# Kernel optimization log

Measured on AMD Instinct MI355X. Metric: run time of the kernel, lower is better.

## Reference

```python
import jax, jax.numpy as jnp
import numpy as np

B, N, D, P, DS = 64, 16, 64, 5, 32
M = N * (N - 1)
TEMP = (DS * P * P) ** 0.5


def conv2d(x, w, b):
    # NCHW conv, stride 1, padding==SAME for k=3/p=1 and k=1/p=0
    y = jax.lax.conv_general_dilated(x, w, (1, 1), 'SAME',
                                     dimension_numbers=('NCHW', 'OIHW', 'NCHW'))
    return y + b[None, :, None, None]


def setup_inputs() -> dict:
    key = jax.random.key(0)
    ks = jax.random.split(key, 10)
    w = lambda k, shape: jax.random.normal(k, shape, jnp.float32) * 0.02
    x = jax.random.normal(ks[0], (B, N, D, P, P), jnp.float32)
    # g_idx: all ordered pairs (i, j) with j != i, plus valid flag 1
    pairs = np.array([(i, j) for i in range(N) for j in range(N) if j != i], dtype=np.int64)
    g = np.concatenate([pairs, np.ones((M, 1), np.int64)], axis=1)  # [M,3]
    g_idx = jnp.tile(jnp.asarray(g)[None], (B, 1, 1))  # [B,M,3]
    return dict(
        x=x, g_idx=g_idx,
        w_rel=w(ks[1], (D, 2 * D, 3, 3)), b_rel=jnp.zeros((D,), jnp.float32),
        w_self=w(ks[2], (D, D, 3, 3)), b_self=jnp.zeros((D,), jnp.float32),
        w_aff=w(ks[3], (D, D, 3, 3)), b_aff=jnp.zeros((D,), jnp.float32),
        w_agg=w(ks[4], (D, 2 * D, 3, 3)), b_agg=jnp.zeros((D,), jnp.float32),
        w_attn=w(ks[5], (DS, D, 1, 1)), b_attn=jnp.zeros((DS,), jnp.float32),
        w_q=w(ks[6], (DS, DS, 3, 3)), b_q=jnp.zeros((DS,), jnp.float32),
        w_k=w(ks[7], (DS, DS, 3, 3)), b_k=jnp.zeros((DS,), jnp.float32),
        gamma=jnp.ones((N, D, P, P), jnp.float32),
        beta=jnp.zeros((N, D, P, P), jnp.float32),
    )


def reference(x, g_idx, w_rel, b_rel, w_self, b_self, w_aff, b_aff,
              w_agg, b_agg, w_attn, b_attn, w_q, b_q, w_k, b_k, gamma, beta):
    s = x
    bsz, n, d, p, _ = x.shape
    # pairwise gather: x1[b, m] == x[b, m % n]
    x1 = jnp.tile(x, (1, n - 1, 1, 1, 1))  # [B, M, D, P, P]
    bidx = jnp.arange(bsz)[:, None]
    y1 = x1[bidx, g_idx[:, :, 0]]  # [B, M, D, P, P]
    y2 = x1[bidx, g_idx[:, :, 1]]
    r = jnp.concatenate([y1, y2], axis=2)  # [B, M, 2D, P, P]
    r = r * g_idx[:, :, 2][:, :, None, None, None].astype(x.dtype)
    r = jax.nn.relu(conv2d(r.reshape(-1, 2 * d, p, p), w_rel, b_rel))
    r = r.reshape(bsz, n, n - 1, d, p, p)
    # attention over objects
    s2d = conv2d(s.reshape(-1, d, p, p), w_attn, b_attn)  # [B*N, DS, P, P]
    q = jax.nn.relu(conv2d(s2d, w_q, b_q)).reshape(bsz, n, -1)
    k = jax.nn.relu(conv2d(s2d, w_k, b_k)).reshape(bsz, n, -1)
    attn = jnp.einsum('bif,bjf->bij', q / TEMP, k)
    sm = jax.nn.softmax(attn, axis=-1)
    self_wts = jnp.diagonal(sm, axis1=1, axis2=2)  # [B, N]
    # off-diagonal weights, per row in ascending column order (matches torch bool-mask view)
    off = jnp.asarray(np.array([[j for j in range(n) if j != i] for i in range(n)], dtype=np.int64))
    rel_wts = jnp.take_along_axis(sm, off[None], axis=2)  # [B, N, N-1]
    r = (rel_wts[:, :, :, None, None, None] * r).sum(axis=2)  # [B, N, D, P, P]
    xs = jax.nn.relu(conv2d(x.reshape(-1, d, p, p), w_self, b_self)).reshape(bsz, n, d, p, p)
    pred = self_wts[:, :, None, None, None] * xs + r
    a = jax.nn.relu(conv2d(pred.reshape(-1, d, p, p), w_aff, b_aff)).reshape(bsz, n, d, p, p)
    a = a + s
    # LayerNorm over [N, D, P, P] per batch element
    mu = a.mean(axis=(1, 2, 3, 4), keepdims=True)
    var = a.var(axis=(1, 2, 3, 4), keepdims=True)
    a = (a - mu) / jnp.sqrt(var + 1e-6) * gamma[None] + beta[None]
    a = jnp.concatenate([a, s], axis=2)  # [B, N, 2D, P, P]
    out = jax.nn.relu(conv2d(a.reshape(-1, 2 * d, p, p), w_agg, b_agg)).reshape(bsz, n, d, p, p)
    return out
```

## Files before the change

### kernel.cpp

```cpp
#include <hip/hip_runtime.h>
#include <hip/hip_bf16.h>

#define DEV static __device__ __forceinline__

typedef short s8v __attribute__((ext_vector_type(8)));
typedef float f16v __attribute__((ext_vector_type(16)));
typedef unsigned short u16;
typedef unsigned int u32;

constexpr int IMG = 1024;
constexpr int IE  = 1600;
constexpr float INV_TEMP = 0.035355339059327376f;

constexpr int WU = 0, WV = 36864, WSELF = 73728, WAFF = 110592,
              WAGA = 147456, WAGS = 184320;
constexpr int WQ = 221184, WK = 230400;
constexpr size_t OFF_Q    = 119808;
constexpr size_t OFF_K    = OFF_Q + 819200;
constexpr size_t OFF_U    = OFF_Q;
constexpr size_t OFF_V    = OFF_Q + 1638400;
constexpr size_t OFF_XS   = OFF_V + 1638400;
constexpr size_t OFF_A    = OFF_XS + 1638400;
constexpr size_t OFF_SM   = OFF_A + 1638400;
constexpr size_t OFF_SUMS = OFF_SM + 16384;
constexpr size_t OFF_WTS  = OFF_SUMS + 128;

DEV u16 f2bf(float f) {
  u32 u = __float_as_uint(f);
  return (u16)((u + 0x7FFF + ((u >> 16) & 1)) >> 16);
}
DEV int xrow(int p) { return (p / 5 + 1) * 8 + (p % 5 + 1); }
DEV int slotOf(int R) { return (3 * (R >> 3) + (R & 7)) & 7; }
DEV f16v zero16() {
  f16v z;
#pragma unroll
  for (int i = 0; i < 16; ++i) z[i] = 0.f;
  return z;
}
DEV void xt_write_pair(u16* xt, int p, int cp, float v0, float v1) {
  int R = xrow(p);
  int chunk = ((cp >> 2) ^ slotOf(R)) & 7;
  u32 u = (u32)f2bf(v0) | ((u32)f2bf(v1) << 16);
  *(u32*)((char*)xt + R * 128 + chunk * 16 + (cp & 3) * 4) = u;
}
DEV void mk_bases(int lane, int bases[9]) {
  int p = lane & 31; if (p > 24) p = 24;
  int hi = lane >> 5;
  int y = p / 5, x = p % 5;
#pragma unroll
  for (int t = 0; t < 9; ++t) {
    int R = (y + t / 3) * 8 + (x + t % 3);
    int sl = slotOf(R);
    bases[t] = R * 128 + (((sl ^ hi) & 7) << 4);
  }
}

__global__ __launch_bounds__(256) void k0_prep(
    const float* __restrict__ w_rel, const float* __restrict__ w_self,
    const float* __restrict__ w_aff, const float* __restrict__ w_agg,
    const float* __restrict__ w_q, const float* __restrict__ w_k,
    const float* __restrict__ w_attn, float* __restrict__ ws) {
  u16* wb = (u16*)ws;
  int idx = blockIdx.x * 256 + threadIdx.x;
  if (idx < 221184) {
    int reg = idx / 36864, w = idx % 36864;
    int o = w / 576, k = w % 576, t = k >> 6, c = k & 63;
    float v;
    switch (reg) {
      case 0:  v = w_rel[(o * 128 + c) * 9 + t]; break;
      case 1:  v = w_rel[(o * 128 + 64 + c) * 9 + t]; break;
      case 2:  v = w_self[(o * 64 + c) * 9 + t]; break;
      case 3:  v = w_aff[(o * 64 + c) * 9 + t]; break;
      case 4:  v = w_agg[(o * 128 + c) * 9 + t]; break;
      default: v = w_agg[(o * 128 + 64 + c) * 9 + t]; break;
    }
    wb[idx] = f2bf(v);
  } else if (idx < 239616) {
    int i2 = idx - 221184;
    int conv = i2 / 9216, r = i2 % 9216;
    int o = r / 288, k = r % 288, t = k >> 5, c = k & 31;
    const float* src = conv ? w_k : w_q;
    wb[idx] = f2bf(src[(o * 32 + c) * 9 + t]);
  } else if (idx < 239616 + 2048) {
    int i2 = idx - 239616;
    int c = i2 >> 5, ds = i2 & 31;
    ws[OFF_WTS + i2] = w_attn[ds * 64 + c];
  }
}

__global__ __launch_bounds__(256, 2) void k1_qk(
    const float* __restrict__ x, const float* __restrict__ b_attn,
    const float* __restrict__ b_q, const float* __restrict__ b_k,
    float* __restrict__ ws) {
  __shared__ float xlin[3200];
  __shared__ float wts[2048];
  __shared__ u16 xt32[2 * 3584];
  const u16* wb = (const u16*)ws;
  int tid = threadIdx.x, lane = tid & 63, wave = tid >> 6, hi = lane >> 5;
  int img0 = blockIdx.x * 2;
  int conv = wave & 1, wimg = wave >> 1;
  int oA = lane & 31;
  const u16* wsrc = wb + (conv ? WK : WQ) + oA * 288 + hi * 8;
  s8v A[18];
#pragma unroll
  for (int s = 0; s < 18; ++s) A[s] = *(const s8v*)(wsrc + s * 16);
  int bases[9]; mk_bases(lane, bases);
  for (int i = tid; i < 3200; i += 256) xlin[i] = x[(size_t)img0 * IE + i];
  for (int i = tid; i < 2048; i += 256) wts[i] = ws[OFF_WTS + i];
  for (int i = tid; i < 3584; i += 256) ((u32*)xt32)[i] = 0;
  __syncthreads();
  if (tid < 200) {
    int im = tid / 100, r = tid % 100, dsg = r / 25, p = r % 25;
    float acc[8];
#pragma unroll
    for (int d = 0; d < 8; ++d) acc[d] = b_attn[dsg * 8 + d];
    const float* xp = &xlin[im * IE + p];
#pragma unroll 4
    for (int c = 0; c < 64; ++c) {
      float xv = xp[c * 25];
      const float* wp = &wts[c * 32 + dsg * 8];
#pragma unroll
      for (int d = 0; d < 8; ++d) acc[d] = fmaf(wp[d], xv, acc[d]);
    }
    s8v pk;
#pragma unroll
    for (int d = 0; d < 8; ++d) pk[d] = (short)f2bf(acc[d]);
    int R = xrow(p);
    int chunk = (dsg ^ slotOf(R)) & 7;
    *(s8v*)((char*)xt32 + im * 7168 + R * 128 + chunk * 16) = pk;
  }
  __syncthreads();
  f16v acc = zero16();
  const char* xb = (const char*)xt32 + wimg * 7168;
#pragma unroll
  for (int s = 0; s < 18; ++s) {
    s8v bfr = *(const s8v*)(xb + (bases[s >> 1] ^ ((s & 1) << 5)));
    acc = __builtin_amdgcn_mfma_f32_32x32x16_bf16(A[s], bfr, acc, 0, 0, 0);
  }
  float* outp = ws + (conv ? OFF_K : OFF_Q) + (size_t)(img0 + wimg) * 800;
  const float* bq = conv ? b_k : b_q;
  int p = lane & 31;
  if (p < 25) {
#pragma unroll
    for (int r = 0; r < 16; ++r) {
      int ol = (r & 3) + 8 * (r >> 2) + 4 * hi;
      outp[ol * 25 + p] = fmaxf(acc[r] + bq[ol], 0.f);
    }
  }
}

__global__ __launch_bounds__(256) void k2_attn(float* __restrict__ ws) {
  __shared__ float kb[16][804];
  __shared__ float att[16][17];
  __shared__ float rowm[16], rowsum[16];
  int b = blockIdx.x, tid = threadIdx.x;
  const float* kg = ws + OFF_K + (size_t)b * 12800;
  for (int i = tid; i < 12800; i += 256) kb[i / 800][i % 800] = kg[i];
  if (tid < 2) ws[OFF_SUMS + b * 2 + tid] = 0.f;
  __syncthreads();
  int i = tid >> 4, j = tid & 15;
  const float* qr = ws + OFF_Q + (size_t)(b * 16 + i) * 800;
  float acc = 0.f;
  for (int f = 0; f < 800; f += 4) {
    float4 a = *(const float4*)(qr + f);
    float4 c = *(const float4*)&kb[j][f];
    acc += a.x * c.x + a.y * c.y + a.z * c.z + a.w * c.w;
  }
  att[i][j] = acc * INV_TEMP;
  __syncthreads();
  if (tid < 16) {
    float m = att[tid][0];
    for (int jj = 1; jj < 16; ++jj) m = fmaxf(m, att[tid][jj]);
    float s = 0.f;
    for (int jj = 0; jj < 16; ++jj) s += expf(att[tid][jj] - m);
    rowm[tid] = m; rowsum[tid] = 1.f / s;
  }
  __syncthreads();
  ws[OFF_SM + (size_t)b * 256 + tid] = expf(att[i][j] - rowm[i]) * rowsum[i];
}

__global__ __launch_bounds__(384, 2) void k3_uvxs(
    const float* __restrict__ x, const float* __restrict__ b_rel,
    const float* __restrict__ b_self, float* __restrict__ ws) {
  __shared__ float xlin[1600];
  __shared__ u16 xt[3584];
  const u16* wb = (const u16*)ws;
  int tid = threadIdx.x, lane = tid & 63, wave = tid >> 6, hi = lane >> 5;
  int conv = wave >> 1, ot = wave & 1;
  int oA = ot * 32 + (lane & 31);
  const u16* wsrc = wb + (conv == 0 ? WU : (conv == 1 ? WV : WSELF)) + oA * 576 + hi * 8;
  s8v A[36];
#pragma unroll
  for (int s = 0; s < 36; ++s) A[s] = *(const s8v*)(wsrc + s * 16);
  int bases[9]; mk_bases(lane, bases);
  for (int i = tid; i < 1792; i += 384) ((u32*)xt)[i] = 0;
  int img0 = blockIdx.x * 4;
  size_t obase = conv == 0 ? OFF_U : (conv == 1 ? OFF_V : OFF_XS);
  for (int im = 0; im < 4; ++im) {
    int img = img0 + im;
    __syncthreads();
    for (int i = tid; i < 1600; i += 384) xlin[i] = x[(size_t)img * IE + i];
    __syncthreads();
    for (int i = tid; i < 800; i += 384) {
      int p = i >> 5, cp = i & 31;
      xt_write_pair(xt, p, cp, xlin[cp * 50 + p], xlin[cp * 50 + 25 + p]);
    }
    __syncthreads();
    f16v acc = zero16();
#pragma unroll
    for (int s = 0; s < 36; ++s) {
      s8v bfr = *(const s8v*)((const char*)xt + (bases[s >> 2] ^ ((s & 3) << 5)));
      acc = __builtin_amdgcn_mfma_f32_32x32x16_bf16(A[s], bfr, acc, 0, 0, 0);
    }
    int p = lane & 31;
    if (p < 25) {
      float* outp = ws + obase + (size_t)img * IE;
#pragma unroll
      for (int r = 0; r < 16; ++r) {
        int ol = ot * 32 + (r & 3) + 8 * (r >> 2) + 4 * hi;
        float v = acc[r];
        if (conv == 1) v += b_rel[ol];
        if (conv == 2) v = fmaxf(v + b_self[ol], 0.f);
        outp[ol * 25 + p] = v;
      }
    }
  }
}

__global__ __launch_bounds__(256, 2) void k5_pred_aff(
    const float* __restrict__ x, const float* __restrict__ b_aff,
    float* __restrict__ ws) {
  __shared__ float predlin[2][1600];
  __shared__ u16 xt[2][3584];
  __shared__ float smr[2][16];
  __shared__ float selfw[2];
  const u16* wb = (const u16*)ws;
  int tid = threadIdx.x, lane = tid & 63, wave = tid >> 6, hi = lane >> 5;
  int img0 = blockIdx.x * 2, bat = img0 >> 4;
  int wimg = wave >> 1, ot = wave & 1;
  int oA = ot * 32 + (lane & 31);
  const u16* wsrc = wb + WAFF + oA * 576 + hi * 8;
  s8v A[36];
#pragma unroll
  for (int s = 0; s < 36; ++s) A[s] = *(const s8v*)(wsrc + s * 16);
  int bases[9]; mk_bases(lane, bases);
  for (int i = tid; i < 3584; i += 256) ((u32*)&xt[0][0])[i] = 0;
  if (tid < 32) { int k = tid >> 4, j = tid & 15; smr[k][j] = ws[OFF_SM + (size_t)(img0 + k) * 16 + j]; }
  if (tid < 2)  { int n = (img0 + tid) & 15; selfw[tid] = ws[OFF_SM + (size_t)(img0 + tid) * 16 + n]; }
  __syncthreads();
  const float* U = ws + OFF_U; const float* V = ws + OFF_V; const float* XS = ws + OFF_XS;
  for (int i4 = tid; i4 < 800; i4 += 256) {
    int im = i4 / 400, e = (i4 % 400) * 4;
    size_t gi = (size_t)(img0 + im) * IE + e;
    float4 uu = *(const float4*)(U + gi);
    float4 xx = *(const float4*)(XS + gi);
    float sw = selfw[im];
    int nk = (img0 + im) & 15;
    float ax = sw * xx.x, ay = sw * xx.y, az = sw * xx.z, aw = sw * xx.w;
#pragma unroll
    for (int j = 0; j < 16; ++j) {
      float wj = (j == nk) ? 0.f : smr[im][j];
      float4 vv = *(const float4*)(V + (size_t)(bat * 16 + j) * IE + e);
      ax = fmaf(wj, fmaxf(uu.x + vv.x, 0.f), ax);
      ay = fmaf(wj, fmaxf(uu.y + vv.y, 0.f), ay);
      az = fmaf(wj, fmaxf(uu.z + vv.z, 0.f), az);
      aw = fmaf(wj, fmaxf(uu.w + vv.w, 0.f), aw);
    }
    *(float4*)&predlin[im][e] = make_float4(ax, ay, az, aw);
  }
  __syncthreads();
  for (int i = tid; i < 1600; i += 256) {
    int im = i / 800, r = i % 800, p = r >> 5, cp = r & 31;
    xt_write_pair(&xt[im][0], p, cp, predlin[im][cp * 50 + p], predlin[im][cp * 50 + 25 + p]);
  }
  __syncthreads();
  f16v acc = zero16();
  const char* xb = (const char*)&xt[wimg][0];
#pragma unroll
  for (int s = 0; s < 36; ++s) {
    s8v bfr = *(const s8v*)(xb + (bases[s >> 2] ^ ((s & 3) << 5)));
    acc = __builtin_amdgcn_mfma_f32_32x32x16_bf16(A[s], bfr, acc, 0, 0, 0);
  }
  int p = lane & 31;
  float s1 = 0.f, s2 = 0.f;
  float* aout = ws + OFF_A + (size_t)(img0 + wimg) * IE;
  const float* xg = x + (size_t)(img0 + wimg) * IE;
  if (p < 25) {
#pragma unroll
    for (int r = 0; r < 16; ++r) {
      int ol = ot * 32 + (r & 3) + 8 * (r >> 2) + 4 * hi;
      float a = fmaxf(acc[r] + b_aff[ol], 0.f) + xg[ol * 25 + p];
      aout[ol * 25 + p] = a;
      s1 += a; s2 = fmaf(a, a, s2);
    }
  }
  for (int off = 32; off; off >>= 1) {
    s1 += __shfl_down(s1, off, 64);
    s2 += __shfl_down(s2, off, 64);
  }
  if (lane == 0) {
    atomicAdd(ws + OFF_SUMS + bat * 2, s1);
    atomicAdd(ws + OFF_SUMS + bat * 2 + 1, s2);
  }
}

__global__ __launch_bounds__(256, 2) void k6_agg(
    const float* __restrict__ x, const float* __restrict__ gamma,
    const float* __restrict__ beta, const float* __restrict__ b_agg,
    float* __restrict__ ws, float* __restrict__ out) {
  __shared__ float alin[2][1600];
  __shared__ float xlin[2][1600];
  __shared__ u16 xta[2][3584];
  __shared__ u16 xtx[2][3584];
  __shared__ float pbuf[4][1024];
  const u16* wb = (const u16*)ws;
  int tid = threadIdx.x, lane = tid & 63, wave = tid >> 6, hi = lane >> 5;
  int img0 = blockIdx.x * 2, bat = img0 >> 4;
  int ot = wave >> 1, h = wave & 1;
  int oA = ot * 32 + (lane & 31);
  const u16* wsrc = wb + (h ? WAGS : WAGA) + oA * 576 + hi * 8;
  s8v A[36];
#pragma unroll
  for (int s = 0; s < 36; ++s) A[s] = *(const s8v*)(wsrc + s * 16);
  int bases[9]; mk_bases(lane, bases);
  float ssum = ws[OFF_SUMS + bat * 2], ssq = ws[OFF_SUMS + bat * 2 + 1];
  float mu = ssum * (1.f / 25600.f);
  float var = ssq * (1.f / 25600.f) - mu * mu;
  float rstd = rsqrtf(var + 1e-6f);
  for (int i = tid; i < 3584; i += 256) { ((u32*)&xta[0][0])[i] = 0; ((u32*)&xtx[0][0])[i] = 0; }
  float* al = &alin[0][0]; float* xl = &xlin[0][0];
  const float* ag = ws + OFF_A + (size_t)img0 * IE;
  const float* xg = x + (size_t)img0 * IE;
  for (int i = tid; i < 3200; i += 256) { al[i] = ag[i]; xl[i] = xg[i]; }
  __syncthreads();
  for (int i = tid; i < 1600; i += 256) {
    int im = i / 800, r = i % 800, p = r >> 5, cp = r & 31;
    int n = (img0 + im) & 15;
    int e0 = cp * 50 + p, e1 = e0 + 25;
    float a0 = al[im * 1600 + e0], a1 = al[im * 1600 + e1];
    float an0 = (a0 - mu) * rstd * gamma[(size_t)n * IE + e0] + beta[(size_t)n * IE + e0];
    float an1 = (a1 - mu) * rstd * gamma[(size_t)n * IE + e1] + beta[(size_t)n * IE + e1];
    xt_write_pair(&xta[im][0], p, cp, an0, an1);
    xt_write_pair(&xtx[im][0], p, cp, xl[im * 1600 + e0], xl[im * 1600 + e1]);
  }
  __syncthreads();
  const char* bsrc = h ? (const char*)&xtx[0][0] : (const char*)&xta[0][0];
  f16v acc0 = zero16(), acc1 = zero16();
#pragma unroll
  for (int s = 0; s < 36; ++s) {
    s8v bfr = *(const s8v*)(bsrc + (bases[s >> 2] ^ ((s & 3) << 5)));
    acc0 = __builtin_amdgcn_mfma_f32_32x32x16_bf16(A[s], bfr, acc0, 0, 0, 0);
  }
#pragma unroll
  for (int s = 0; s < 36; ++s) {
    s8v bfr = *(const s8v*)(bsrc + 7168 + (bases[s >> 2] ^ ((s & 3) << 5)));
    acc1 = __builtin_amdgcn_mfma_f32_32x32x16_bf16(A[s], bfr, acc1, 0, 0, 0);
  }
  int p = lane & 31;
  if (h == 1) {
#pragma unroll
    for (int r = 0; r < 16; ++r) {
      int ol = (r & 3) + 8 * (r >> 2) + 4 * hi;
      pbuf[0 + ot][ol * 32 + p] = acc0[r];
      pbuf[2 + ot][ol * 32 + p] = acc1[r];
    }
  }
  __syncthreads();
  if (h == 0 && p < 25) {
#pragma unroll
    for (int r = 0; r < 16; ++r) {
      int ol = (r & 3) + 8 * (r >> 2) + 4 * hi;
      int o = ot * 32 + ol;
      float v0 = acc0[r] + pbuf[0 + ot][ol * 32 + p] + b_agg[o];
      float v1 = acc1[r] + pbuf[2 + ot][ol * 32 + p] + b_agg[o];
      out[(size_t)(img0 + 0) * IE + o * 25 + p] = fmaxf(v0, 0.f);
      out[(size_t)(img0 + 1) * IE + o * 25 + p] = fmaxf(v1, 0.f);
    }
  }
}

extern "C" void kernel_launch(void* const* d_in, const int* in_sizes, int n_in,
                              void* d_out, int out_size, void* d_ws,
                              size_t ws_size, hipStream_t stream) {
  const float* x      = (const float*)d_in[0];
  const float* w_rel  = (const float*)d_in[2];
  const float* b_rel  = (const float*)d_in[3];
  const float* w_self = (const float*)d_in[4];
  const float* b_self = (const float*)d_in[5];
  const float* w_aff  = (const float*)d_in[6];
  const float* b_aff  = (const float*)d_in[7];
  const float* w_agg  = (const float*)d_in[8];
  const float* b_agg  = (const float*)d_in[9];
  const float* w_attn = (const float*)d_in[10];
  const float* b_attn = (const float*)d_in[11];
  const float* w_q    = (const float*)d_in[12];
  const float* b_q    = (const float*)d_in[13];
  const float* w_k    = (const float*)d_in[14];
  const float* b_k    = (const float*)d_in[15];
  const float* gamma  = (const float*)d_in[16];
  const float* beta   = (const float*)d_in[17];
  float* ws  = (float*)d_ws;
  float* out = (float*)d_out;

  k0_prep<<<944, 256, 0, stream>>>(w_rel, w_self, w_aff, w_agg, w_q, w_k, w_attn, ws);
  k1_qk<<<IMG / 2, 256, 0, stream>>>(x, b_attn, b_q, b_k, ws);
  k2_attn<<<64, 256, 0, stream>>>(ws);
  k3_uvxs<<<IMG / 4, 384, 0, stream>>>(x, b_rel, b_self, ws);
  k5_pred_aff<<<IMG / 2, 256, 0, stream>>>(x, b_aff, ws);
  k6_agg<<<IMG / 2, 256, 0, stream>>>(x, gamma, beta, b_agg, ws, out);
}
```

Measured before the change: 206.9 us.

## Use MFMA for attn 1x1 conv, widen attention kernel, shrink per-block work in k3/k6

The 1x1 attention projection in k1 moves from scalar FMA loops over fp32 shared weights to bf16 MFMA using pre-converted weights. k2 uses 1024 threads, with four threads per (i,j) dot product combined by shuffles. k3 processes two images per block instead of four, and k6 processes one image per block instead of two, so both launch more blocks. These are separate changes aimed at more parallelism and tensor-core use, at the cost of bf16 rounding in the attention projection and more weight reloads per image.

```diff
diff --git a/kernel.cpp b/kernel.cpp
--- a/kernel.cpp
+++ b/kernel.cpp
@@ -15,7 +15,8 @@
 constexpr int WU = 0, WV = 36864, WSELF = 73728, WAFF = 110592,
               WAGA = 147456, WAGS = 184320;
 constexpr int WQ = 221184, WK = 230400;
-constexpr size_t OFF_Q    = 119808;
+constexpr int WATT = 239616;
+constexpr size_t OFF_Q    = 120832;
 constexpr size_t OFF_K    = OFF_Q + 819200;
 constexpr size_t OFF_U    = OFF_Q;
 constexpr size_t OFF_V    = OFF_Q + 1638400;
@@ -23,7 +24,6 @@
 constexpr size_t OFF_A    = OFF_XS + 1638400;
 constexpr size_t OFF_SM   = OFF_A + 1638400;
 constexpr size_t OFF_SUMS = OFF_SM + 16384;
-constexpr size_t OFF_WTS  = OFF_SUMS + 128;
 
 DEV u16 f2bf(float f) {
   u32 u = __float_as_uint(f);
@@ -81,10 +81,8 @@
     int o = r / 288, k = r % 288, t = k >> 5, c = k & 31;
     const float* src = conv ? w_k : w_q;
     wb[idx] = f2bf(src[(o * 32 + c) * 9 + t]);
-  } else if (idx < 239616 + 2048) {
-    int i2 = idx - 239616;
-    int c = i2 >> 5, ds = i2 & 31;
-    ws[OFF_WTS + i2] = w_attn[ds * 64 + c];
+  } else if (idx < 241664) {
+    wb[idx] = f2bf(w_attn[idx - 239616]);
   }
 }
 
@@ -93,53 +91,60 @@
     const float* __restrict__ b_q, const float* __restrict__ b_k,
     float* __restrict__ ws) {
   __shared__ float xlin[3200];
-  __shared__ float wts[2048];
-  __shared__ u16 xt32[2 * 3584];
+  __shared__ u16 xtx[2 * 3584];
+  __shared__ u16 xts[2 * 3584];
+  __shared__ float batt[32];
   const u16* wb = (const u16*)ws;
   int tid = threadIdx.x, lane = tid & 63, wave = tid >> 6, hi = lane >> 5;
   int img0 = blockIdx.x * 2;
   int conv = wave & 1, wimg = wave >> 1;
   int oA = lane & 31;
   const u16* wsrc = wb + (conv ? WK : WQ) + oA * 288 + hi * 8;
-  s8v A[18];
-#pragma unroll
-  for (int s = 0; s < 18; ++s) A[s] = *(const s8v*)(wsrc + s * 16);
+  s8v Aq[18];
+#pragma unroll
+  for (int s = 0; s < 18; ++s) Aq[s] = *(const s8v*)(wsrc + s * 16);
+  const u16* wa = wb + WATT + oA * 64 + hi * 8;
+  s8v As[4];
+#pragma unroll
+  for (int s = 0; s < 4; ++s) As[s] = *(const s8v*)(wa + s * 16);
   int bases[9]; mk_bases(lane, bases);
   for (int i = tid; i < 3200; i += 256) xlin[i] = x[(size_t)img0 * IE + i];
-  for (int i = tid; i < 2048; i += 256) wts[i] = ws[OFF_WTS + i];
-  for (int i = tid; i < 3584; i += 256) ((u32*)xt32)[i] = 0;
-  __syncthreads();
-  if (tid < 200) {
-    int im = tid / 100, r = tid % 100, dsg = r / 25, p = r % 25;
-    float acc[8];
-#pragma unroll
-    for (int d = 0; d < 8; ++d) acc[d] = b_attn[dsg * 8 + d];
-    const float* xp = &xlin[im * IE + p];
-#pragma unroll 4
-    for (int c = 0; c < 64; ++c) {
-      float xv = xp[c * 25];
-      const float* wp = &wts[c * 32 + dsg * 8];
-#pragma unroll
-      for (int d = 0; d < 8; ++d) acc[d] = fmaf(wp[d], xv, acc[d]);
-    }
-    s8v pk;
-#pragma unroll
-    for (int d = 0; d < 8; ++d) pk[d] = (short)f2bf(acc[d]);
-    int R = xrow(p);
-    int chunk = (dsg ^ slotOf(R)) & 7;
-    *(s8v*)((char*)xt32 + im * 7168 + R * 128 + chunk * 16) = pk;
+  if (tid < 32) batt[tid] = b_attn[tid];
+  for (int i = tid; i < 3584; i += 256) { ((u32*)xtx)[i] = 0; ((u32*)xts)[i] = 0; }
+  __syncthreads();
+  for (int i = tid; i < 1600; i += 256) {
+    int im = i / 800, r = i % 800, p = r >> 5, cp = r & 31;
+    xt_write_pair(xtx + im * 3584, p, cp,
+                  xlin[im * 1600 + cp * 50 + p], xlin[im * 1600 + cp * 50 + 25 + p]);
+  }
+  __syncthreads();
+  f16v sacc = zero16();
+  const char* xbx = (const char*)xtx + wimg * 7168;
+#pragma unroll
+  for (int s = 0; s < 4; ++s) {
+    s8v bfr = *(const s8v*)(xbx + (bases[4] ^ (s << 5)));
+    sacc = __builtin_amdgcn_mfma_f32_32x32x16_bf16(As[s], bfr, sacc, 0, 0, 0);
+  }
+  int p = lane & 31;
+  if (conv == 0 && p < 25) {
+#pragma unroll
+    for (int a = 0; a < 8; ++a) {
+      int r0 = 2 * a;
+      int ds0 = (r0 & 3) + 8 * (r0 >> 2) + 4 * hi;
+      xt_write_pair(xts + wimg * 3584, p, ds0 >> 1,
+                    sacc[r0] + batt[ds0], sacc[r0 + 1] + batt[ds0 + 1]);
+    }
   }
   __syncthreads();
   f16v acc = zero16();
-  const char* xb = (const char*)xt32 + wimg * 7168;
+  const char* xbs = (const char*)xts + wimg * 7168;
 #pragma unroll
   for (int s = 0; s < 18; ++s) {
-    s8v bfr = *(const s8v*)(xb + (bases[s >> 1] ^ ((s & 1) << 5)));
-    acc = __builtin_amdgcn_mfma_f32_32x32x16_bf16(A[s], bfr, acc, 0, 0, 0);
+    s8v bfr = *(const s8v*)(xbs + (bases[s >> 1] ^ ((s & 1) << 5)));
+    acc = __builtin_amdgcn_mfma_f32_32x32x16_bf16(Aq[s], bfr, acc, 0, 0, 0);
   }
   float* outp = ws + (conv ? OFF_K : OFF_Q) + (size_t)(img0 + wimg) * 800;
   const float* bq = conv ? b_k : b_q;
-  int p = lane & 31;
   if (p < 25) {
 #pragma unroll
     for (int r = 0; r < 16; ++r) {
@@ -149,24 +154,27 @@
   }
 }
 
-__global__ __launch_bounds__(256) void k2_attn(float* __restrict__ ws) {
+__global__ __launch_bounds__(1024) void k2_attn(float* __restrict__ ws) {
   __shared__ float kb[16][804];
   __shared__ float att[16][17];
   __shared__ float rowm[16], rowsum[16];
   int b = blockIdx.x, tid = threadIdx.x;
   const float* kg = ws + OFF_K + (size_t)b * 12800;
-  for (int i = tid; i < 12800; i += 256) kb[i / 800][i % 800] = kg[i];
+  for (int i = tid; i < 12800; i += 1024) kb[i / 800][i % 800] = kg[i];
   if (tid < 2) ws[OFF_SUMS + b * 2 + tid] = 0.f;
   __syncthreads();
-  int i = tid >> 4, j = tid & 15;
+  int pair = tid >> 2, sub = tid & 3;
+  int i = pair >> 4, j = pair & 15;
   const float* qr = ws + OFF_Q + (size_t)(b * 16 + i) * 800;
   float acc = 0.f;
-  for (int f = 0; f < 800; f += 4) {
+  for (int f = sub * 4; f < 800; f += 16) {
     float4 a = *(const float4*)(qr + f);
     float4 c = *(const float4*)&kb[j][f];
     acc += a.x * c.x + a.y * c.y + a.z * c.z + a.w * c.w;
   }
-  att[i][j] = acc * INV_TEMP;
+  acc += __shfl_xor(acc, 1, 64);
+  acc += __shfl_xor(acc, 2, 64);
+  if (sub == 0) att[i][j] = acc * INV_TEMP;
   __syncthreads();
   if (tid < 16) {
     float m = att[tid][0];
@@ -176,7 +184,10 @@
     rowm[tid] = m; rowsum[tid] = 1.f / s;
   }
   __syncthreads();
-  ws[OFF_SM + (size_t)b * 256 + tid] = expf(att[i][j] - rowm[i]) * rowsum[i];
+  if (tid < 256) {
+    int ii = tid >> 4, jj = tid & 15;
+    ws[OFF_SM + (size_t)b * 256 + tid] = expf(att[ii][jj] - rowm[ii]) * rowsum[ii];
+  }
 }
 
 __global__ __launch_bounds__(384, 2) void k3_uvxs(
@@ -194,9 +205,9 @@
   for (int s = 0; s < 36; ++s) A[s] = *(const s8v*)(wsrc + s * 16);
   int bases[9]; mk_bases(lane, bases);
   for (int i = tid; i < 1792; i += 384) ((u32*)xt)[i] = 0;
-  int img0 = blockIdx.x * 4;
+  int img0 = blockIdx.x * 2;
   size_t obase = conv == 0 ? OFF_U : (conv == 1 ? OFF_V : OFF_XS);
-  for (int im = 0; im < 4; ++im) {
+  for (int im = 0; im < 2; ++im) {
     int img = img0 + im;
     __syncthreads();
     for (int i = tid; i < 1600; i += 384) xlin[i] = x[(size_t)img * IE + i];
@@ -308,14 +319,14 @@
     const float* __restrict__ x, const float* __restrict__ gamma,
     const float* __restrict__ beta, const float* __restrict__ b_agg,
     float* __restrict__ ws, float* __restrict__ out) {
-  __shared__ float alin[2][1600];
-  __shared__ float xlin[2][1600];
-  __shared__ u16 xta[2][3584];
-  __shared__ u16 xtx[2][3584];
-  __shared__ float pbuf[4][1024];
+  __shared__ float alin[1600];
+  __shared__ float xlin[1600];
+  __shared__ u16 xta[3584];
+  __shared__ u16 xtx[3584];
+  __shared__ float pbuf[2][1024];
   const u16* wb = (const u16*)ws;
   int tid = threadIdx.x, lane = tid & 63, wave = tid >> 6, hi = lane >> 5;
-  int img0 = blockIdx.x * 2, bat = img0 >> 4;
+  int img = blockIdx.x, bat = img >> 4, n = img & 15;
   int ot = wave >> 1, h = wave & 1;
   int oA = ot * 32 + (lane & 31);
   const u16* wsrc = wb + (h ? WAGS : WAGA) + oA * 576 + hi * 8;
@@ -327,42 +338,33 @@
   float mu = ssum * (1.f / 25600.f);
   float var = ssq * (1.f / 25600.f) - mu * mu;
   float rstd = rsqrtf(var + 1e-6f);
-  for (int i = tid; i < 3584; i += 256) { ((u32*)&xta[0][0])[i] = 0; ((u32*)&xtx[0][0])[i] = 0; }
-  float* al = &alin[0][0]; float* xl = &xlin[0][0];
-  const float* ag = ws + OFF_A + (size_t)img0 * IE;
-  const float* xg = x + (size_t)img0 * IE;
-  for (int i = tid; i < 3200; i += 256) { al[i] = ag[i]; xl[i] = xg[i]; }
-  __syncthreads();
-  for (int i = tid; i < 1600; i += 256) {
-    int im = i / 800, r = i % 800, p = r >> 5, cp = r & 31;
-    int n = (img0 + im) & 15;
+  for (int i = tid; i < 1792; i += 256) { ((u32*)xta)[i] = 0; ((u32*)xtx)[i] = 0; }
+  const float* ag = ws + OFF_A + (size_t)img * IE;
+  const float* xg = x + (size_t)img * IE;
+  for (int i = tid; i < 1600; i += 256) { alin[i] = ag[i]; xlin[i] = xg[i]; }
+  __syncthreads();
+  for (int i = tid; i < 800; i += 256) {
+    int p = i >> 5, cp = i & 31;
     int e0 = cp * 50 + p, e1 = e0 + 25;
-    float a0 = al[im * 1600 + e0], a1 = al[im * 1600 + e1];
-    float an0 = (a0 - mu) * rstd * gamma[(size_t)n * IE + e0] + beta[(size_t)n * IE + e0];
-    float an1 = (a1 - mu) * rstd * gamma[(size_t)n * IE + e1] + beta[(size_t)n * IE + e1];
-    xt_write_pair(&xta[im][0], p, cp, an0, an1);
-    xt_write_pair(&xtx[im][0], p, cp, xl[im * 1600 + e0], xl[im * 1600 + e1]);
-  }
-  __syncthreads();
-  const char* bsrc = h ? (const char*)&xtx[0][0] : (const char*)&xta[0][0];
-  f16v acc0 = zero16(), acc1 = zero16();
+    float an0 = (alin[e0] - mu) * rstd * gamma[(size_t)n * IE + e0] + beta[(size_t)n * IE + e0];
+    float an1 = (alin[e1] - mu) * rstd * gamma[(size_t)n * IE + e1] + beta[(size_t)n * IE + e1];
+    xt_write_pair(xta, p, cp, an0, an1);
+    xt_write_pair(xtx, p, cp, xlin[e0], xlin[e1]);
+  }
+  __syncthreads();
+  const char* bsrc = h ? (const char*)xtx : (const char*)xta;
+  f16v acc = zero16();
 #pragma unroll
   for (int s = 0; s < 36; ++s) {
     s8v bfr = *(const s8v*)(bsrc + (bases[s >> 2] ^ ((s & 3) << 5)));
-    acc0 = __builtin_amdgcn_mfma_f32_32x32x16_bf16(A[s], bfr, acc0, 0, 0, 0);
-  }
-#pragma unroll
-  for (int s = 0; s < 36; ++s) {
-    s8v bfr = *(const s8v*)(bsrc + 7168 + (bases[s >> 2] ^ ((s & 3) << 5)));
-    acc1 = __builtin_amdgcn_mfma_f32_32x32x16_bf16(A[s], bfr, acc1, 0, 0, 0);
+    acc = __builtin_amdgcn_mfma_f32_32x32x16_bf16(A[s], bfr, acc, 0, 0, 0);
   }
   int p = lane & 31;
   if (h == 1) {
 #pragma unroll
     for (int r = 0; r < 16; ++r) {
       int ol = (r & 3) + 8 * (r >> 2) + 4 * hi;
-      pbuf[0 + ot][ol * 32 + p] = acc0[r];
-      pbuf[2 + ot][ol * 32 + p] = acc1[r];
+      pbuf[ot][ol * 32 + p] = acc[r];
     }
   }
   __syncthreads();
@@ -371,10 +373,8 @@
     for (int r = 0; r < 16; ++r) {
       int ol = (r & 3) + 8 * (r >> 2) + 4 * hi;
       int o = ot * 32 + ol;
-      float v0 = acc0[r] + pbuf[0 + ot][ol * 32 + p] + b_agg[o];
-      float v1 = acc1[r] + pbuf[2 + ot][ol * 32 + p] + b_agg[o];
-      out[(size_t)(img0 + 0) * IE + o * 25 + p] = fmaxf(v0, 0.f);
-      out[(size_t)(img0 + 1) * IE + o * 25 + p] = fmaxf(v1, 0.f);
+      float v = acc[r] + pbuf[ot][ol * 32 + p] + b_agg[o];
+      out[(size_t)img * IE + o * 25 + p] = fmaxf(v, 0.f);
     }
   }
 }
@@ -404,8 +404,8 @@
 
   k0_prep<<<944, 256, 0, stream>>>(w_rel, w_self, w_aff, w_agg, w_q, w_k, w_attn, ws);
   k1_qk<<<IMG / 2, 256, 0, stream>>>(x, b_attn, b_q, b_k, ws);
-  k2_attn<<<64, 256, 0, stream>>>(ws);
-  k3_uvxs<<<IMG / 4, 384, 0, stream>>>(x, b_rel, b_self, ws);
+  k2_attn<<<64, 1024, 0, stream>>>(ws);
+  k3_uvxs<<<IMG / 2, 384, 0, stream>>>(x, b_rel, b_self, ws);
   k5_pred_aff<<<IMG / 2, 256, 0, stream>>>(x, b_aff, ws);
-  k6_agg<<<IMG / 2, 256, 0, stream>>>(x, gamma, beta, b_agg, ws, out);
-}
+  k6_agg<<<IMG, 256, 0, stream>>>(x, gamma, beta, b_agg, ws, out);
+}
```

New measurement: 223.6 us. 1.08x slower.
